# Kernel tuning notes

Measured on AMD Instinct MI355X. Metric: run time of the kernel, lower is better.

## Reference

```python
import math
import jax, jax.numpy as jnp
import numpy as np

B, S, H = 2, 2048, 1024
NH = 16
HD = H // NH            # 64
ROT = int(HD * 0.25)    # 16
QKV_SLOTS = 1024
PROJ_SLOTS = 1024
FFN_SLOTS = 4096
EPS = 1e-5


def gelu_l2_norm(x, axis=-1):
    # F.gelu (exact erf) then L2-normalize and rescale by sqrt(dim)
    g = jax.nn.gelu(x, approximate=False)
    n = jnp.linalg.norm(g, ord=2, axis=axis, keepdims=True)
    return g / n * math.sqrt(g.shape[axis])


def layer_norm(x, w, b):
    mu = jnp.mean(x, axis=-1, keepdims=True)
    var = jnp.mean(jnp.square(x - mu), axis=-1, keepdims=True)
    return (x - mu) * jax.lax.rsqrt(var + EPS) * w + b


def pattention(x, key_tok, val_tok):
    # [.., in] @ [slots, in]^T -> [.., slots]; NOTE: scale MULTIPLIES (as in source)
    aw = jnp.einsum('bsh,ph->bsp', x, key_tok) * math.sqrt(x.shape[-1])
    aw = gelu_l2_norm(aw, axis=-1)
    return jnp.einsum('bsp,pd->bsd', aw, val_tok)


def rotary_cos_sin(seq_len, rot_dim, base=10000.0):
    inv_freq = 1.0 / (base ** (jnp.arange(0, rot_dim, 2, dtype=jnp.float32) / rot_dim))
    t = jnp.arange(seq_len, dtype=jnp.float32)
    freqs = jnp.einsum('s,d->sd', t, inv_freq)           # [S, rot/2]
    emb = jnp.concatenate([freqs, freqs], axis=-1)       # [S, rot]
    return jnp.cos(emb), jnp.sin(emb)


def rotate_half(x):
    x1, x2 = jnp.split(x, 2, axis=-1)
    return jnp.concatenate([-x2, x1], axis=-1)


def setup_inputs() -> dict:
    key = jax.random.key(0)
    ks = jax.random.split(key, 12)
    p = lambda k, shape: jax.random.normal(k, shape, dtype=jnp.float32) * 0.02
    return {
        'x': jax.random.normal(ks[0], (B, S, H), dtype=jnp.float32),
        'ln1_w': jnp.ones((H,), jnp.float32), 'ln1_b': jnp.zeros((H,), jnp.float32),
        'ln2_w': jnp.ones((H,), jnp.float32), 'ln2_b': jnp.zeros((H,), jnp.float32),
        'q_key': p(ks[1], (QKV_SLOTS, H)), 'q_val': p(ks[2], (QKV_SLOTS, H)),
        'k_key': p(ks[3], (QKV_SLOTS, H)), 'k_val': p(ks[4], (QKV_SLOTS, H)),
        'v_key': p(ks[5], (QKV_SLOTS, H)), 'v_val': p(ks[6], (QKV_SLOTS, H)),
        'proj_key': p(ks[7], (PROJ_SLOTS, H)), 'proj_val': p(ks[8], (PROJ_SLOTS, H)),
        'ffn_key': p(ks[9], (FFN_SLOTS, H)), 'ffn_val': p(ks[10], (FFN_SLOTS, H)),
    }


def reference(x, ln1_w, ln1_b, ln2_w, ln2_b, q_key, q_val, k_key, k_val,
              v_key, v_val, proj_key, proj_val, ffn_key, ffn_val):
    residual = x
    xn = layer_norm(x, ln1_w, ln1_b)
    q = pattention(xn, q_key, q_val).reshape(B, S, NH, HD)
    k = pattention(xn, k_key, k_val).reshape(B, S, NH, HD)
    v = pattention(xn, v_key, v_val).reshape(B, S, NH, HD)

    cos, sin = rotary_cos_sin(S, ROT)          # [S, ROT]
    cos = cos[None, :, None, :]
    sin = sin[None, :, None, :]
    q_rot, q_pass = q[..., :ROT], q[..., ROT:]
    k_rot, k_pass = k[..., :ROT], k[..., ROT:]
    q_rot = q_rot * cos + rotate_half(q_rot) * sin
    k_rot = k_rot * cos + rotate_half(k_rot) * sin
    q = jnp.concatenate([q_rot, q_pass], axis=-1).transpose(0, 2, 1, 3)  # [B,NH,S,HD]
    k = jnp.concatenate([k_rot, k_pass], axis=-1).transpose(0, 2, 1, 3)
    v = v.transpose(0, 2, 1, 3)

    scale = math.sqrt(HD)
    causal = jnp.triu(jnp.ones((S, S), dtype=bool), k=1)
    attn_mask = jnp.where(causal, jnp.float32(-10000.0), jnp.float32(0.0))
    aw = jnp.einsum('bhqd,bhkd->bhqk', q, k) / scale + attn_mask
    aw = gelu_l2_norm(aw, axis=-1)
    o = jnp.einsum('bhqk,bhkd->bhqd', aw, v)
    o = o.transpose(0, 2, 1, 3).reshape(B, S, H)

    x = residual + pattention(o, proj_key, proj_val)
    residual = x
    x = residual + pattention(layer_norm(x, ln2_w, ln2_b), ffn_key, ffn_val)
    return x
```

## Files before the change

### kernel.cpp

```cpp
#include <hip/hip_runtime.h>

typedef __bf16 bf16x8 __attribute__((ext_vector_type(8)));
typedef float f32x4 __attribute__((ext_vector_type(4)));
typedef unsigned short u16;

__device__ __forceinline__ float b2f(u16 u) {
  union { unsigned int i; float f; } v; v.i = ((unsigned int)u) << 16; return v.f;
}
__device__ __forceinline__ u16 f2b(float f) {
  union { float f; unsigned int i; } v; v.f = f;
  unsigned int x = v.i;
  x += 0x7fffu + ((x >> 16) & 1u);
  return (u16)(x >> 16);
}
__device__ __forceinline__ float gelu_f(float x) {
  float x2 = x * x;
  float p = x * (1.5957691216f + 0.0713548162f * x2);
  float e = __expf(p);
  float r = __builtin_amdgcn_rcpf(1.0f + e);
  return x - x * r;
}
__device__ __forceinline__ void async16(const u16* g, u16* l) {
  __builtin_amdgcn_global_load_lds(
      (const __attribute__((address_space(1))) void*)g,
      (__attribute__((address_space(3))) void*)l, 16, 0, 0);
}
__device__ __forceinline__ void swz(int& bn, int& bm, int& bz) {
  int gx = (int)gridDim.x, gy = (int)gridDim.y;
  int flat = (int)(blockIdx.x + gridDim.x * (blockIdx.y + gridDim.y * blockIdx.z));
  int seq = flat >> 3;
  int nbm = gy >> 3;
  bm = (flat & 7) * nbm + seq % nbm;
  int rest = seq / nbm;
  bn = rest % gx;
  bz = rest / gx;
}

union U4 { uint4 u; u16 s[8]; };

__global__ __launch_bounds__(256) void cvt9_kernel(
    const float* __restrict__ qk, const float* __restrict__ kk,
    const float* __restrict__ vk, const float* __restrict__ pk,
    const float* __restrict__ fk, u16* __restrict__ w, float* __restrict__ ssqz) {
  int z = blockIdx.y;
  int i = blockIdx.x * 256 + threadIdx.x;
  if (z == 8) {
    if (i < 20480) ssqz[i] = 0.f;
    return;
  }
  const float* in = (z == 0) ? qk : (z == 1) ? kk : (z == 2) ? vk : (z == 3) ? pk
                    : fk + (size_t)(z - 4) * 1048576;
  u16* o = w + (size_t)z * 1048576;
  float4 f = ((const float4*)in)[i];
  ushort4 s;
  s.x = f2b(f.x); s.y = f2b(f.y); s.z = f2b(f.z); s.w = f2b(f.w);
  ((ushort4*)o)[i] = s;
}

__global__ __launch_bounds__(256) void cvtT8_kernel(
    const float* __restrict__ qv, const float* __restrict__ kv,
    const float* __restrict__ vv, const float* __restrict__ pv,
    const float* __restrict__ fv, u16* __restrict__ valsT, u16* __restrict__ fvT) {
  __shared__ float t[32][33];
  int z = blockIdx.z;
  const float* in; u16* o; int Rout, rowoff;
  if (z < 4) {
    in = (z == 0) ? qv : (z == 1) ? kv : (z == 2) ? vv : pv;
    o = valsT + (size_t)z * 1048576; Rout = 1024; rowoff = 0;
  } else {
    in = fv + (size_t)(z - 4) * 1048576;
    o = fvT; Rout = 4096; rowoff = (z - 4) * 1024;
  }
  int bc = blockIdx.x, br = blockIdx.y;
  int tid = threadIdx.x;
  int r = tid >> 5, cc = tid & 31;
  #pragma unroll
  for (int i = 0; i < 4; ++i)
    t[r + i * 8][cc] = in[(size_t)(br * 32 + r + i * 8) * 1024 + bc * 32 + cc];
  __syncthreads();
  #pragma unroll
  for (int i = 0; i < 4; ++i)
    o[(size_t)(bc * 32 + r + i * 8) * Rout + rowoff + br * 32 + cc] = f2b(t[cc][r + i * 8]);
}

__global__ __launch_bounds__(256) void ln_kernel(const float* __restrict__ x,
    const float* __restrict__ w, const float* __restrict__ b, u16* __restrict__ out) {
  int wv = threadIdx.x >> 6, lane = threadIdx.x & 63;
  int row = blockIdx.x * 4 + wv;
  const float* xr = x + (size_t)row * 1024;
  float4 v[4];
  float s = 0.f, s2 = 0.f;
  #pragma unroll
  for (int i = 0; i < 4; ++i) {
    v[i] = ((const float4*)xr)[lane + 64 * i];
    s += v[i].x + v[i].y + v[i].z + v[i].w;
    s2 += v[i].x * v[i].x + v[i].y * v[i].y + v[i].z * v[i].z + v[i].w * v[i].w;
  }
  #pragma unroll
  for (int m = 1; m < 64; m <<= 1) { s += __shfl_xor(s, m); s2 += __shfl_xor(s2, m); }
  float mu = s * (1.0f / 1024.0f);
  float inv = rsqrtf(s2 * (1.0f / 1024.0f) - mu * mu + 1e-5f);
  u16* orow = out + (size_t)row * 1024;
  #pragma unroll
  for (int i = 0; i < 4; ++i) {
    int c = (lane + 64 * i) * 4;
    ushort4 o;
    o.x = f2b((v[i].x - mu) * inv * w[c]     + b[c]);
    o.y = f2b((v[i].y - mu) * inv * w[c + 1] + b[c + 1]);
    o.z = f2b((v[i].z - mu) * inv * w[c + 2] + b[c + 2]);
    o.w = f2b((v[i].w - mu) * inv * w[c + 3] + b[c + 3]);
    ((ushort4*)orow)[lane + 64 * i] = o;
  }
}


template <int TM>
__global__ __launch_bounds__(256) void gemm_key(
    const u16* __restrict__ A, size_t sAz,
    const u16* __restrict__ B, size_t sBz,
    u16* __restrict__ C, size_t sCz,
    float* __restrict__ ssqb, size_t sSz,
    int N, int K, float alpha) {
  constexpr int AI = TM / 32;
  __shared__ __align__(16) u16 As[2][TM * 32];
  __shared__ __align__(16) u16 Bs[2][128 * 32];
  int bn, bm, bz;
  swz(bn, bm, bz);
  const u16* Ab = A + (size_t)bz * sAz + (size_t)bm * TM * K;
  const u16* Bb = B + (size_t)bz * sBz + (size_t)bn * 128 * K;
  int tid = threadIdx.x, lane = tid & 63, wv = tid >> 6;
  int quad = lane >> 4, l16 = lane & 15;
  int lr = lane >> 2;
  int lcs = ((lane & 3) ^ ((lane >> 3) & 3)) * 8;
  int rq = quad ^ ((l16 >> 1) & 3);
  int wm = wv >> 1, wn = wv & 1;
  int RB = wm * (TM / 2), CB = wn * 64;
  f32x4 zero = {0.f, 0.f, 0.f, 0.f};
  f32x4 acc[AI][4];
  #pragma unroll
  for (int i = 0; i < AI; ++i)
    #pragma unroll
    for (int j = 0; j < 4; ++j) acc[i][j] = zero;
  #pragma unroll
  for (int t = 0; t < TM / 64; ++t) {
    int ia = wv * (TM / 64) + t;
    async16(Ab + (size_t)(ia * 16 + lr) * K + lcs, &As[0][ia * 512]);
  }
  #pragma unroll
  for (int t = 0; t < 2; ++t) {
    int ib = wv * 2 + t;
    async16(Bb + (size_t)(ib * 16 + lr) * K + lcs, &Bs[0][ib * 512]);
  }
  for (int k0 = 0, cur = 0; k0 < K; k0 += 32, cur ^= 1) {
    __syncthreads();
    if (k0 + 32 < K) {
      #pragma unroll
      for (int t = 0; t < TM / 64; ++t) {
        int ia = wv * (TM / 64) + t;
        async16(Ab + (size_t)(ia * 16 + lr) * K + k0 + 32 + lcs, &As[cur ^ 1][ia * 512]);
      }
      #pragma unroll
      for (int t = 0; t < 2; ++t) {
        int ib = wv * 2 + t;
        async16(Bb + (size_t)(ib * 16 + lr) * K + k0 + 32 + lcs, &Bs[cur ^ 1][ib * 512]);
      }
    }
    bf16x8 af[AI], bf[4];
    #pragma unroll
    for (int i = 0; i < AI; ++i)
      af[i] = *(const bf16x8*)&As[cur][(RB + i * 16 + l16) * 32 + rq * 8];
    #pragma unroll
    for (int j = 0; j < 4; ++j)
      bf[j] = *(const bf16x8*)&Bs[cur][(CB + j * 16 + l16) * 32 + rq * 8];
    #pragma unroll
    for (int i = 0; i < AI; ++i)
      #pragma unroll
      for (int j = 0; j < 4; ++j)
        acc[i][j] = __builtin_amdgcn_mfma_f32_16x16x32_bf16(af[i], bf[j], acc[i][j], 0, 0, 0);
  }
  #pragma unroll
  for (int i = 0; i < AI; ++i) {
    int rbase = bm * TM + RB + i * 16 + quad * 4;
    float srow[4] = {0.f, 0.f, 0.f, 0.f};
    #pragma unroll
    for (int j = 0; j < 4; ++j) {
      int c = bn * 128 + CB + j * 16 + l16;
      #pragma unroll
      for (int reg = 0; reg < 4; ++reg) {
        float g = gelu_f(acc[i][j][reg] * alpha);
        srow[reg] += g * g;
        C[(size_t)bz * sCz + (size_t)(rbase + reg) * N + c] = f2b(g);
      }
    }
    #pragma unroll
    for (int reg = 0; reg < 4; ++reg) {
      float s = srow[reg];
      s += __shfl_xor(s, 1); s += __shfl_xor(s, 2);
      s += __shfl_xor(s, 4); s += __shfl_xor(s, 8);
      if (l16 == 0) atomicAdd(&ssqb[bz * sSz + rbase + reg], s);
    }
  }
}

template <int TM, int MODE, bool ROT>
__global__ __launch_bounds__(256) void gemm_val(
    const u16* __restrict__ A, size_t sAz,
    const u16* __restrict__ B, size_t sBz,
    void* __restrict__ C, size_t sCz,
    const float* __restrict__ ssqb, size_t sSz,
    int N, int K, int kzs, int klen, float sqrtP, const float* __restrict__ res) {
  constexpr int AI = TM / 32;
  __shared__ __align__(16) u16 As[2][TM * 32];
  __shared__ __align__(16) u16 Bs[2][128 * 32];
  int bn, bm, bz;
  swz(bn, bm, bz);
  const u16* Ab = A + (size_t)bz * sAz + (size_t)bm * TM * K;
  const u16* Bb = B + (size_t)bz * sBz + (size_t)bn * 128 * K;
  int tid = threadIdx.x, lane = tid & 63, wv = tid >> 6;
  int quad = lane >> 4, l16 = lane & 15;
  int lr = lane >> 2;
  int lcs = ((lane & 3) ^ ((lane >> 3) & 3)) * 8;
  int rq = quad ^ ((l16 >> 1) & 3);
  int wm = wv >> 1, wn = wv & 1;
  int RB = wm * (TM / 2), CB = wn * 64;
  f32x4 zero = {0.f, 0.f, 0.f, 0.f};
  f32x4 acc[AI][4];
  #pragma unroll
  for (int i = 0; i < AI; ++i)
    #pragma unroll
    for (int j = 0; j < 4; ++j) acc[i][j] = zero;
  int kb0 = bz * kzs;
  #pragma unroll
  for (int t = 0; t < TM / 64; ++t) {
    int ia = wv * (TM / 64) + t;
    async16(Ab + (size_t)(ia * 16 + lr) * K + kb0 + lcs, &As[0][ia * 512]);
  }
  #pragma unroll
  for (int t = 0; t < 2; ++t) {
    int ib = wv * 2 + t;
    async16(Bb + (size_t)(ib * 16 + lr) * K + kb0 + lcs, &Bs[0][ib * 512]);
  }
  for (int k0 = kb0, cur = 0; k0 < kb0 + klen; k0 += 32, cur ^= 1) {
    __syncthreads();
    if (k0 + 32 < kb0 + klen) {
      #pragma unroll
      for (int t = 0; t < TM / 64; ++t) {
        int ia = wv * (TM / 64) + t;
        async16(Ab + (size_t)(ia * 16 + lr) * K + k0 + 32 + lcs, &As[cur ^ 1][ia * 512]);
      }
      #pragma unroll
      for (int t = 0; t < 2; ++t) {
        int ib = wv * 2 + t;
        async16(Bb + (size_t)(ib * 16 + lr) * K + k0 + 32 + lcs, &Bs[cur ^ 1][ib * 512]);
      }
    }
    bf16x8 af[AI], bf[4];
    #pragma unroll
    for (int i = 0; i < AI; ++i)
      af[i] = *(const bf16x8*)&As[cur][(RB + i * 16 + l16) * 32 + rq * 8];
    #pragma unroll
    for (int j = 0; j < 4; ++j)
      bf[j] = *(const bf16x8*)&Bs[cur][(CB + j * 16 + l16) * 32 + rq * 8];
    #pragma unroll
    for (int i = 0; i < AI; ++i)
      #pragma unroll
      for (int j = 0; j < 4; ++j)
        acc[i][j] = __builtin_amdgcn_mfma_f32_16x16x32_bf16(af[i], bf[j], acc[i][j], 0, 0, 0);
  }
  #pragma unroll
  for (int i = 0; i < AI; ++i) {
    int rbase = bm * TM + RB + i * 16 + quad * 4;
    float sc[4];
    if (MODE < 2) {
      #pragma unroll
      for (int reg = 0; reg < 4; ++reg)
        sc[reg] = sqrtP * rsqrtf(ssqb[bz * sSz + rbase + reg]);
    }
    #pragma unroll
    for (int j = 0; j < 4; ++j) {
      int c = bn * 128 + CB + j * 16 + l16;
      #pragma unroll
      for (int reg = 0; reg < 4; ++reg) {
        float v = acc[i][j][reg];
        size_t idx = (size_t)(rbase + reg) * N + c;
        if (MODE == 0) {
          float vs = v * sc[reg];
          if (ROT && j == 0) {
            float prt = __shfl_xor(vs, 8);
            if (bz < 2) {
              int seq = (rbase + reg) & 2047;
              float fr = exp2f((float)(l16 & 7) * -1.66096404744368f);
              float ang = (float)seq * fr;
              float c_ = __cosf(ang), s_ = __sinf(ang);
              vs = (l16 < 8) ? (vs * c_ - prt * s_) : (vs * c_ + prt * s_);
            }
          }
          ((u16*)C)[(size_t)bz * sCz + idx] = f2b(vs);
        } else if (MODE == 1) {
          ((float*)C)[idx] = v * sc[reg] + res[idx];
        } else {
          ((float*)C)[(size_t)bz * sCz + idx] = v;
        }
      }
    }
  }
}

__global__ __launch_bounds__(256) void vt_kernel(const u16* __restrict__ vb,
                                                 u16* __restrict__ vT) {
  __shared__ __align__(16) u16 T[64][72];
  int st = blockIdx.x, bh = blockIdx.y;
  int b = bh >> 4, h = bh & 15;
  int tid = threadIdx.x;
  #pragma unroll
  for (int i = 0; i < 2; ++i) {
    int l = tid + 256 * i;
    int s = l >> 3, dc = l & 7;
    *(uint4*)&T[s][dc * 8] =
        *(const uint4*)(vb + (size_t)(b * 2048 + st * 64 + s) * 1024 + h * 64 + dc * 8);
  }
  __syncthreads();
  #pragma unroll
  for (int i = 0; i < 2; ++i) {
    int l = tid + 256 * i;
    int d = l >> 3, scid = l & 7;
    int blk = (scid >> 2) * 32;
    int qq = (scid & 3) * 4;
    U4 u;
    #pragma unroll
    for (int j = 0; j < 8; ++j)
      u.s[j] = T[blk + (j >> 2) * 16 + qq + (j & 3)][d];
    *(uint4*)(vT + ((size_t)bh * 64 + d) * 2048 + st * 64 + scid * 8) = u.u;
  }
}

__global__ __launch_bounds__(256) void attn_kernel(
    const u16* __restrict__ qb, const u16* __restrict__ kb,
    const u16* __restrict__ vT, u16* __restrict__ ob) {
  __shared__ __align__(16) u16 Qs[64 * 64];
  __shared__ __align__(16) u16 Ks[2][64 * 64];
  __shared__ __align__(16) u16 Vts[2][64 * 64];
  int bh = blockIdx.x;
  int qt = 31 - (int)blockIdx.y;
  int b = bh >> 4, h = bh & 15;
  const u16* qp = qb + (size_t)b * 2048 * 1024 + h * 64;
  const u16* kp = kb + (size_t)b * 2048 * 1024 + h * 64;
  const u16* vp = vT + (size_t)bh * 64 * 2048;
  int tid = threadIdx.x, lane = tid & 63, wv = tid >> 6;
  int quad = lane >> 4, l16 = lane & 15;
  int lr8 = lane >> 3;
  int lc8s = ((lane & 7) ^ lr8) * 8;
  int rx = (l16 & 7) << 3;
  int MR = wv * 16;
  int nkt = qt + 1;
  #pragma unroll
  for (int t = 0; t < 2; ++t) {
    int idx = wv * 2 + t;
    async16(qp + (size_t)(qt * 64 + idx * 8 + lr8) * 1024 + lc8s, &Qs[idx * 512]);
    async16(kp + (size_t)(idx * 8 + lr8) * 1024 + lc8s, &Ks[0][idx * 512]);
    async16(vp + (size_t)(idx * 8 + lr8) * 2048 + lc8s, &Vts[0][idx * 512]);
  }
  f32x4 zero = {0.f, 0.f, 0.f, 0.f};
  f32x4 oacc[4];
  #pragma unroll
  for (int dn = 0; dn < 4; ++dn) oacc[dn] = zero;
  float ssql = 0.f;
  bf16x8 bq0 = {}, bq1 = {};
  for (int kt = 0, cur = 0; kt < nkt; ++kt, cur ^= 1) {
    __syncthreads();
    if (kt == 0) {
      bq0 = *(const bf16x8*)&Qs[((MR + l16) * 64 + quad * 8) ^ rx];
      bq1 = *(const bf16x8*)&Qs[((MR + l16) * 64 + 32 + quad * 8) ^ rx];
    }
    if (kt + 1 < nkt) {
      #pragma unroll
      for (int t = 0; t < 2; ++t) {
        int idx = wv * 2 + t;
        async16(kp + (size_t)((kt + 1) * 64 + idx * 8 + lr8) * 1024 + lc8s, &Ks[cur ^ 1][idx * 512]);
        async16(vp + (size_t)(idx * 8 + lr8) * 2048 + (kt + 1) * 64 + lc8s, &Vts[cur ^ 1][idx * 512]);
      }
    }
    bool dg = (kt == qt);
    #pragma unroll
    for (int kc = 0; kc < 2; ++kc) {
      bf16x8 pf;
      #pragma unroll
      for (int snh = 0; snh < 2; ++snh) {
        int sn = kc * 2 + snh;
        bf16x8 ak0 = *(const bf16x8*)&Ks[cur][((sn * 16 + l16) * 64 + quad * 8) ^ rx];
        bf16x8 ak1 = *(const bf16x8*)&Ks[cur][((sn * 16 + l16) * 64 + 32 + quad * 8) ^ rx];
        f32x4 st = zero;
        st = __builtin_amdgcn_mfma_f32_16x16x32_bf16(ak0, bq0, st, 0, 0, 0);
        st = __builtin_amdgcn_mfma_f32_16x16x32_bf16(ak1, bq1, st, 0, 0, 0);
        #pragma unroll
        for (int r = 0; r < 4; ++r) {
          float gl = gelu_f(st[r] * 0.125f);
          if (dg && (sn * 16 + quad * 4 + r > MR + l16)) gl = 0.f;
          ssql += gl * gl;
          pf[snh * 4 + r] = (__bf16)gl;
        }
      }
      #pragma unroll
      for (int dn = 0; dn < 4; ++dn) {
        bf16x8 bv = *(const bf16x8*)&Vts[cur][((dn * 16 + l16) * 64 + kc * 32 + quad * 8) ^ rx];
        oacc[dn] = __builtin_amdgcn_mfma_f32_16x16x32_bf16(pf, bv, oacc[dn], 0, 0, 0);
      }
    }
  }
  ssql += __shfl_xor(ssql, 16);
  ssql += __shfl_xor(ssql, 32);
  float sc = 45.254834f * rsqrtf(ssql);
  #pragma unroll
  for (int dn = 0; dn < 4; ++dn)
    #pragma unroll
    for (int r = 0; r < 4; ++r) {
      float scr = __shfl(sc, quad * 4 + r);
      int row = qt * 64 + MR + quad * 4 + r;
      int col = h * 64 + dn * 16 + l16;
      ob[(size_t)(b * 2048 + row) * 1024 + col] = f2b(oacc[dn][r] * scr);
    }
}

__global__ __launch_bounds__(256) void fin_kernel(
    const float* __restrict__ p0, const float* __restrict__ p1,
    const float* __restrict__ x1, const float* __restrict__ ssqf,
    float* __restrict__ out) {
  int row = blockIdx.x, t = threadIdx.x;
  float s = 64.0f * rsqrtf(ssqf[row]);
  size_t base = (size_t)row * 1024 + t * 4;
  float4 a = *(const float4*)(p0 + base);
  float4 b = *(const float4*)(p1 + base);
  float4 r = *(const float4*)(x1 + base);
  float4 o;
  o.x = r.x + s * (a.x + b.x); o.y = r.y + s * (a.y + b.y);
  o.z = r.z + s * (a.z + b.z); o.w = r.w + s * (a.w + b.w);
  *(float4*)(out + base) = o;
}

extern "C" void kernel_launch(void* const* d_in, const int* in_sizes, int n_in,
                              void* d_out, int out_size, void* d_ws, size_t ws_size,
                              hipStream_t stream) {
  const float* x    = (const float*)d_in[0];
  const float* ln1w = (const float*)d_in[1];
  const float* ln1b = (const float*)d_in[2];
  const float* ln2w = (const float*)d_in[3];
  const float* ln2b = (const float*)d_in[4];
  const float* qk   = (const float*)d_in[5];
  const float* qv   = (const float*)d_in[6];
  const float* kk   = (const float*)d_in[7];
  const float* kv   = (const float*)d_in[8];
  const float* vk   = (const float*)d_in[9];
  const float* vv   = (const float*)d_in[10];
  const float* pk   = (const float*)d_in[11];
  const float* pv   = (const float*)d_in[12];
  const float* fk   = (const float*)d_in[13];
  const float* fv   = (const float*)d_in[14];
  float* out = (float*)d_out;

  const size_t M1 = 1048576;
  u16* w = (u16*)d_ws;
  u16* wkeys  = w;
  u16* wpk    = w + 3 * M1;
  u16* wfk    = w + 4 * M1;
  u16* wvalsT = w + 8 * M1;
  u16* wpvT   = w + 11 * M1;
  u16* wfvT   = w + 12 * M1;
  u16* xn     = w + 16 * M1;
  u16* gq     = w + 20 * M1;
  u16* ob     = w + 20 * M1;
  u16* vT     = w + 24 * M1;
  u16* gp     = w + 28 * M1;
  u16* gf     = w + 20 * M1;
  u16* qb     = w + 36 * M1;
  u16* kb     = w + 40 * M1;
  u16* vb     = w + 44 * M1;
  float* ssq_qkv  = (float*)(w + 48 * M1);
  float* ssq_proj = ssq_qkv + 12288;
  float* ssq_ffn  = ssq_qkv + 16384;
  float* x1 = (float*)(w + 52 * M1);
  float* p0 = (float*)w;
  float* p1 = (float*)(w + 36 * M1);

  dim3 blk(256);
  cvt9_kernel<<<dim3(1024, 9), blk, 0, stream>>>(qk, kk, vk, pk, fk, w, ssq_qkv);
  cvtT8_kernel<<<dim3(32, 32, 8), blk, 0, stream>>>(qv, kv, vv, pv, fv, wvalsT, wfvT);

  ln_kernel<<<1024, blk, 0, stream>>>(x, ln1w, ln1b, xn);
  gemm_key<128><<<dim3(8, 32, 3), blk, 0, stream>>>(
      xn, 0, wkeys, M1, gq, 4 * M1, ssq_qkv, 4096, 1024, 1024, 32.0f);
  gemm_val<128, 0, true><<<dim3(8, 32, 3), blk, 0, stream>>>(
      gq, 4 * M1, wvalsT, M1, qb, 4 * M1, ssq_qkv, 4096, 1024, 1024, 0, 1024, 32.0f, nullptr);

  vt_kernel<<<dim3(32, 32), blk, 0, stream>>>(vb, vT);
  attn_kernel<<<dim3(32, 32), blk, 0, stream>>>(qb, kb, vT, ob);

  gemm_key<64><<<dim3(8, 64, 1), blk, 0, stream>>>(
      ob, 0, wpk, 0, gp, 0, ssq_proj, 0, 1024, 1024, 32.0f);
  gemm_val<64, 1, false><<<dim3(8, 64, 1), blk, 0, stream>>>(
      gp, 0, wpvT, 0, x1, 0, ssq_proj, 0, 1024, 1024, 0, 1024, 32.0f, x);

  ln_kernel<<<1024, blk, 0, stream>>>(x1, ln2w, ln2b, xn);
  gemm_key<128><<<dim3(32, 32, 1), blk, 0, stream>>>(
      xn, 0, wfk, 0, gf, 0, ssq_ffn, 0, 4096, 1024, 32.0f);
  gemm_val<128, 2, false><<<dim3(8, 32, 2), blk, 0, stream>>>(
      gf, 0, wfvT, 0, p0, 18 * M1, ssq_ffn, 0, 1024, 4096, 2048, 2048, 0.0f, nullptr);
  fin_kernel<<<4096, blk, 0, stream>>>(p0, p1, x1, ssq_ffn, out);
}
```

Measured before the change: 429.1 us.

## Triple-buffer LDS loads in pattention GEMMs with partial vmcnt waits

Both pattention GEMM kernels move from double to triple buffering of the A/B tiles in LDS. Loads are issued two k-steps ahead, and each iteration waits only until its own stage has landed (s_waitcnt vmcnt) before a raw barrier, so global-to-LDS copies overlap more with MFMA work. The cost is 50% more LDS per block, which may lower occupancy. Correctness now depends on the hand-counted vmcnt and on K being a multiple of 32 with at least two tiles.

```diff
diff --git a/kernel.cpp b/kernel.cpp
--- a/kernel.cpp
+++ b/kernel.cpp
@@ -122,8 +122,9 @@
     float* __restrict__ ssqb, size_t sSz,
     int N, int K, float alpha) {
   constexpr int AI = TM / 32;
-  __shared__ __align__(16) u16 As[2][TM * 32];
-  __shared__ __align__(16) u16 Bs[2][128 * 32];
+  constexpr int G = TM / 64 + 2;
+  __shared__ __align__(16) u16 As[3][TM * 32];
+  __shared__ __align__(16) u16 Bs[3][128 * 32];
   int bn, bm, bz;
   swz(bn, bm, bz);
   const u16* Ab = A + (size_t)bz * sAz + (size_t)bm * TM * K;
@@ -135,36 +136,33 @@
   int rq = quad ^ ((l16 >> 1) & 3);
   int wm = wv >> 1, wn = wv & 1;
   int RB = wm * (TM / 2), CB = wn * 64;
+  auto STAGE = [&](int k0, int buf) {
+    #pragma unroll
+    for (int t = 0; t < TM / 64; ++t) {
+      int ia = wv * (TM / 64) + t;
+      async16(Ab + (size_t)(ia * 16 + lr) * K + k0 + lcs, &As[buf][ia * 512]);
+    }
+    #pragma unroll
+    for (int t = 0; t < 2; ++t) {
+      int ib = wv * 2 + t;
+      async16(Bb + (size_t)(ib * 16 + lr) * K + k0 + lcs, &Bs[buf][ib * 512]);
+    }
+  };
   f32x4 zero = {0.f, 0.f, 0.f, 0.f};
   f32x4 acc[AI][4];
   #pragma unroll
   for (int i = 0; i < AI; ++i)
     #pragma unroll
     for (int j = 0; j < 4; ++j) acc[i][j] = zero;
-  #pragma unroll
-  for (int t = 0; t < TM / 64; ++t) {
-    int ia = wv * (TM / 64) + t;
-    async16(Ab + (size_t)(ia * 16 + lr) * K + lcs, &As[0][ia * 512]);
-  }
-  #pragma unroll
-  for (int t = 0; t < 2; ++t) {
-    int ib = wv * 2 + t;
-    async16(Bb + (size_t)(ib * 16 + lr) * K + lcs, &Bs[0][ib * 512]);
-  }
-  for (int k0 = 0, cur = 0; k0 < K; k0 += 32, cur ^= 1) {
-    __syncthreads();
-    if (k0 + 32 < K) {
-      #pragma unroll
-      for (int t = 0; t < TM / 64; ++t) {
-        int ia = wv * (TM / 64) + t;
-        async16(Ab + (size_t)(ia * 16 + lr) * K + k0 + 32 + lcs, &As[cur ^ 1][ia * 512]);
-      }
-      #pragma unroll
-      for (int t = 0; t < 2; ++t) {
-        int ib = wv * 2 + t;
-        async16(Bb + (size_t)(ib * 16 + lr) * K + k0 + 32 + lcs, &Bs[cur ^ 1][ib * 512]);
-      }
-    }
+  int NT = K >> 5;
+  STAGE(0, 0);
+  STAGE(32, 1);
+  int cur = 0;
+  for (int t = 0; t < NT; ++t) {
+    if (t + 1 < NT) asm volatile("s_waitcnt vmcnt(%0)" :: "i"(G) : "memory");
+    else            asm volatile("s_waitcnt vmcnt(0)" ::: "memory");
+    __builtin_amdgcn_s_barrier();
+    __builtin_amdgcn_sched_barrier(0);
     bf16x8 af[AI], bf[4];
     #pragma unroll
     for (int i = 0; i < AI; ++i)
@@ -172,11 +170,16 @@
     #pragma unroll
     for (int j = 0; j < 4; ++j)
       bf[j] = *(const bf16x8*)&Bs[cur][(CB + j * 16 + l16) * 32 + rq * 8];
+    if (t + 2 < NT) {
+      int nb = cur + 2; if (nb >= 3) nb -= 3;
+      STAGE((t + 2) * 32, nb);
+    }
     #pragma unroll
     for (int i = 0; i < AI; ++i)
       #pragma unroll
       for (int j = 0; j < 4; ++j)
         acc[i][j] = __builtin_amdgcn_mfma_f32_16x16x32_bf16(af[i], bf[j], acc[i][j], 0, 0, 0);
+    cur = (cur == 2) ? 0 : cur + 1;
   }
   #pragma unroll
   for (int i = 0; i < AI; ++i) {
@@ -210,8 +213,9 @@
     const float* __restrict__ ssqb, size_t sSz,
     int N, int K, int kzs, int klen, float sqrtP, const float* __restrict__ res) {
   constexpr int AI = TM / 32;
-  __shared__ __align__(16) u16 As[2][TM * 32];
-  __shared__ __align__(16) u16 Bs[2][128 * 32];
+  constexpr int G = TM / 64 + 2;
+  __shared__ __align__(16) u16 As[3][TM * 32];
+  __shared__ __align__(16) u16 Bs[3][128 * 32];
   int bn, bm, bz;
   swz(bn, bm, bz);
   const u16* Ab = A + (size_t)bz * sAz + (size_t)bm * TM * K;
@@ -223,37 +227,34 @@
   int rq = quad ^ ((l16 >> 1) & 3);
   int wm = wv >> 1, wn = wv & 1;
   int RB = wm * (TM / 2), CB = wn * 64;
+  int kb0 = bz * kzs;
+  auto STAGE = [&](int k0, int buf) {
+    #pragma unroll
+    for (int t = 0; t < TM / 64; ++t) {
+      int ia = wv * (TM / 64) + t;
+      async16(Ab + (size_t)(ia * 16 + lr) * K + kb0 + k0 + lcs, &As[buf][ia * 512]);
+    }
+    #pragma unroll
+    for (int t = 0; t < 2; ++t) {
+      int ib = wv * 2 + t;
+      async16(Bb + (size_t)(ib * 16 + lr) * K + kb0 + k0 + lcs, &Bs[buf][ib * 512]);
+    }
+  };
   f32x4 zero = {0.f, 0.f, 0.f, 0.f};
   f32x4 acc[AI][4];
   #pragma unroll
   for (int i = 0; i < AI; ++i)
     #pragma unroll
     for (int j = 0; j < 4; ++j) acc[i][j] = zero;
-  int kb0 = bz * kzs;
-  #pragma unroll
-  for (int t = 0; t < TM / 64; ++t) {
-    int ia = wv * (TM / 64) + t;
-    async16(Ab + (size_t)(ia * 16 + lr) * K + kb0 + lcs, &As[0][ia * 512]);
-  }
-  #pragma unroll
-  for (int t = 0; t < 2; ++t) {
-    int ib = wv * 2 + t;
-    async16(Bb + (size_t)(ib * 16 + lr) * K + kb0 + lcs, &Bs[0][ib * 512]);
-  }
-  for (int k0 = kb0, cur = 0; k0 < kb0 + klen; k0 += 32, cur ^= 1) {
-    __syncthreads();
-    if (k0 + 32 < kb0 + klen) {
-      #pragma unroll
-      for (int t = 0; t < TM / 64; ++t) {
-        int ia = wv * (TM / 64) + t;
-        async16(Ab + (size_t)(ia * 16 + lr) * K + k0 + 32 + lcs, &As[cur ^ 1][ia * 512]);
-      }
-      #pragma unroll
-      for (int t = 0; t < 2; ++t) {
-        int ib = wv * 2 + t;
-        async16(Bb + (size_t)(ib * 16 + lr) * K + k0 + 32 + lcs, &Bs[cur ^ 1][ib * 512]);
-      }
-    }
+  int NT = klen >> 5;
+  STAGE(0, 0);
+  STAGE(32, 1);
+  int cur = 0;
+  for (int t = 0; t < NT; ++t) {
+    if (t + 1 < NT) asm volatile("s_waitcnt vmcnt(%0)" :: "i"(G) : "memory");
+    else            asm volatile("s_waitcnt vmcnt(0)" ::: "memory");
+    __builtin_amdgcn_s_barrier();
+    __builtin_amdgcn_sched_barrier(0);
     bf16x8 af[AI], bf[4];
     #pragma unroll
     for (int i = 0; i < AI; ++i)
@@ -261,11 +262,16 @@
     #pragma unroll
     for (int j = 0; j < 4; ++j)
       bf[j] = *(const bf16x8*)&Bs[cur][(CB + j * 16 + l16) * 32 + rq * 8];
+    if (t + 2 < NT) {
+      int nb = cur + 2; if (nb >= 3) nb -= 3;
+      STAGE((t + 2) * 32, nb);
+    }
     #pragma unroll
     for (int i = 0; i < AI; ++i)
       #pragma unroll
       for (int j = 0; j < 4; ++j)
         acc[i][j] = __builtin_amdgcn_mfma_f32_16x16x32_bf16(af[i], bf[j], acc[i][j], 0, 0, 0);
+    cur = (cur == 2) ? 0 : cur + 1;
   }
   #pragma unroll
   for (int i = 0; i < AI; ++i) {
```

After: 409.2 us. 4.6% less time.
